# Kernel tuning notes

Hardware: AMD Instinct MI355X
Metric: run time of the kernel (lower is better)

Reference implementation:

```python
import jax, jax.numpy as jnp
import numpy as np

TAU_MIN, TAU_MAX = 5.0, 50.0
BOOST = 3.2
DECO_RATE = 0.01

B, I, F, Q = 4096, 1024, 2048, 4

def setup_inputs() -> dict:
    key = jax.random.key(0)
    ks = jax.random.split(key, 12)
    return {
        "inputs": jax.random.normal(ks[0], (B, I), jnp.float32),
        "hidden_state": jax.random.normal(ks[1], (B, F), jnp.float32),
        "W_in": jax.random.normal(ks[2], (I, F), jnp.float32) / np.sqrt(I),
        "b_in": jnp.zeros((F,), jnp.float32),
        "amp_real": jax.random.normal(ks[3], (F, Q), jnp.float32) * 0.1,
        "amp_imag": jax.random.normal(ks[4], (F, Q), jnp.float32) * 0.1,
        "phase": jax.random.uniform(ks[5], (F, Q), jnp.float32, 0.0, 2 * np.pi),
        "primary": jax.random.normal(ks[6], (F, F), jnp.float32) / np.sqrt(F),
        "ent_mat": jax.random.normal(ks[7], (F, F), jnp.float32) / np.sqrt(F),
        "corr": jax.random.uniform(ks[8], (F,), jnp.float32, 0.0, 0.7),
        "W_tau": jax.random.uniform(ks[9], (F, F), jnp.float32, 0.0, 0.1) / np.sqrt(F),
        "b_tau": jnp.zeros((F,), jnp.float32),
        "W_dec": jax.random.uniform(ks[10], (F, F), jnp.float32, 0.0, 0.5) / np.sqrt(F),
        "b_dec": jnp.zeros((F,), jnp.float32),
        "time_step": 1,
    }

def reference(inputs, hidden_state, W_in, b_in, amp_real, amp_imag, phase,
              primary, ent_mat, corr, W_tau, b_tau, W_dec, b_dec, time_step):
    t = jnp.float32(time_step)
    batch = inputs.shape[0]
    feats = hidden_state.shape[1]

    # input projection: [B,I] @ [I,F]
    x_proj = inputs @ W_in + b_in

    # quantum superposition state (batch-independent, [F,Q] params)
    ph = phase + t * 0.1
    real_c = amp_real * jnp.cos(ph)          # [F,Q]
    imag_c = amp_imag * jnp.sin(ph)          # [F,Q]
    sup_r = real_c.sum(-1)                    # [F]
    sup_i = imag_c.sum(-1)                    # [F]
    prob_amp = real_c ** 2 + imag_c ** 2      # [F,Q]
    q_state = sup_r * jnp.exp(-sup_i ** 2)    # [F]
    q_state_b = jnp.broadcast_to(q_state, (batch, feats))
    prob_amp_b = jnp.broadcast_to(prob_amp, (batch,) + prob_amp.shape)

    # entangled recurrent connections: two F x F matmuls
    ent_rec = hidden_state @ primary + (hidden_state @ ent_mat) * corr

    # quantum time constants
    tau_raw = q_state_b @ W_tau + b_tau
    tau_q = (TAU_MIN + (TAU_MAX - TAU_MIN) * jax.nn.sigmoid(tau_raw)) / BOOST

    # decoherence gate
    deco = jax.nn.sigmoid(q_state_b @ W_dec + b_dec)
    coherent = jnp.exp(-DECO_RATE * t)

    classical = jnp.tanh(x_proj + ent_rec)
    quantum_act = q_state_b * deco * coherent
    combined = classical + quantum_act

    dx_dt = (-hidden_state + combined) / tau_q
    dt_q = 0.1 / BOOST
    new_hidden = hidden_state + dt_q * dx_dt

    # diagnostics
    d_amp = jnp.mean(prob_amp_b, axis=-1)          # [B,F]
    d_coh = coherent
    d_ent = jnp.mean(jnp.abs(ent_rec))
    d_dec = jnp.mean(deco)
    d_tau = jnp.mean(tau_q)
    return (new_hidden, d_amp, d_coh, d_ent, d_dec, d_tau)
```

## Files before the change

kernel.cpp:

```cpp
#include <hip/hip_runtime.h>
#include <hip/hip_bf16.h>

#define BD 4096
#define ID 1024
#define FD 2048

typedef __bf16 v8bf __attribute__((ext_vector_type(8)));
typedef float  v4f  __attribute__((ext_vector_type(4)));

struct alignas(8) bf4 { __hip_bfloat16 x, y, z, w; };

__device__ inline __hip_bfloat16 bf(float f) { return __float2bfloat16(f); }
__device__ inline float sig(float x) { return 1.f / (1.f + expf(-x)); }

__device__ inline void gload16(const __hip_bfloat16* g, __hip_bfloat16* l) {
  __builtin_amdgcn_global_load_lds(
      (const __attribute__((address_space(1))) void*)g,
      (__attribute__((address_space(3))) void*)l, 16, 0, 0);
}

__global__ void k_prep_q(const float* ar, const float* ai, const float* ph,
                         const int* tstep, float* qs, float* pamp,
                         float* scal, float* tau_raw, float* dec_raw) {
  int j = blockIdx.x * 256 + threadIdx.x;
  if (j < 4) scal[j] = 0.f;
  if (j < FD) { tau_raw[j] = 0.f; dec_raw[j] = 0.f; }
  if (j >= FD) return;
  float t = (float)tstep[0];
  float4 a = ((const float4*)ar)[j];
  float4 b = ((const float4*)ai)[j];
  float4 p = ((const float4*)ph)[j];
  float sr = 0.f, si = 0.f, pm = 0.f;
  {
    float c, s, rc, ic;
    c = cosf(p.x + 0.1f * t); s = sinf(p.x + 0.1f * t);
    rc = a.x * c; ic = b.x * s; sr += rc; si += ic; pm += rc * rc + ic * ic;
    c = cosf(p.y + 0.1f * t); s = sinf(p.y + 0.1f * t);
    rc = a.y * c; ic = b.y * s; sr += rc; si += ic; pm += rc * rc + ic * ic;
    c = cosf(p.z + 0.1f * t); s = sinf(p.z + 0.1f * t);
    rc = a.z * c; ic = b.z * s; sr += rc; si += ic; pm += rc * rc + ic * ic;
    c = cosf(p.w + 0.1f * t); s = sinf(p.w + 0.1f * t);
    rc = a.w * c; ic = b.w * s; sr += rc; si += ic; pm += rc * rc + ic * ic;
  }
  qs[j] = sr * expf(-si * si);
  pamp[j] = 0.25f * pm;
}

__global__ void k_cast(const float* s1, __hip_bfloat16* d1, int n1,
                       const float* s2, __hip_bfloat16* d2) {
  int i = blockIdx.x * blockDim.x + threadIdx.x;
  const float* src = s1; __hip_bfloat16* dst = d1;
  if (i >= n1) { i -= n1; src = s2; dst = d2; }
  float4 v = ((const float4*)src)[i];
  bf4 o{bf(v.x), bf(v.y), bf(v.z), bf(v.w)};
  ((bf4*)dst)[i] = o;
}

__global__ void k_tcast(const float* src, const float* src2, const float* corr,
                        __hip_bfloat16* dst, int R, int C, int useM) {
  __shared__ float t[32][33];
  int tx = threadIdx.x, ty = threadIdx.y;
  int x = blockIdx.x * 32 + tx;
  int yb = blockIdx.y * 32;
  float cr = useM ? corr[x] : 0.f;
#pragma unroll
  for (int j = 0; j < 4; j++) {
    int y = yb + ty + j * 8;
    float v = src[(size_t)y * C + x];
    if (useM) v += src2[(size_t)y * C + x] * cr;
    t[ty + j * 8][tx] = v;
  }
  __syncthreads();
#pragma unroll
  for (int j = 0; j < 4; j++) {
    int orow = blockIdx.x * 32 + ty + j * 8;
    int ocol = yb + tx;
    dst[(size_t)orow * R + ocol] = bf(t[tx][ty + j * 8]);
  }
}

__global__ void k_matvec(const float* qs, const float* Wt, const float* Wd,
                         float* tau_raw, float* dec_raw) {
  int j = blockIdx.x * 256 + threadIdx.x;
  int i0 = blockIdx.y * 128;
  const float* W = blockIdx.z ? Wd : Wt;
  float* out = blockIdx.z ? dec_raw : tau_raw;
  __shared__ float q[128];
  if (threadIdx.x < 128) q[threadIdx.x] = qs[i0 + threadIdx.x];
  __syncthreads();
  float acc = 0.f;
#pragma unroll 8
  for (int i = 0; i < 128; i++) acc = fmaf(q[i], W[(size_t)(i0 + i) * FD + j], acc);
  atomicAdd(&out[j], acc);
}

__global__ void k_post(const float* tau_raw, const float* dec_raw, const float* qs,
                       const float* b_tau, const float* b_dec, const int* tstep,
                       float* s_arr, float* qact, float* scal) {
  int j = blockIdx.x * 256 + threadIdx.x;
  float t = (float)tstep[0];
  float coh = expf(-0.01f * t);
  float tq = (5.f + 45.f * sig(tau_raw[j] + b_tau[j])) / 3.2f;
  s_arr[j] = 0.03125f / tq;
  float dec = sig(dec_raw[j] + b_dec[j]);
  qact[j] = qs[j] * dec * coh;
  float tsum = tq, dsum = dec;
  for (int off = 32; off; off >>= 1) {
    tsum += __shfl_down(tsum, off);
    dsum += __shfl_down(dsum, off);
  }
  __shared__ float rt[4], rd[4];
  int w = threadIdx.x >> 6;
  if ((threadIdx.x & 63) == 0) { rt[w] = tsum; rd[w] = dsum; }
  __syncthreads();
  if (threadIdx.x == 0) {
    atomicAdd(&scal[1], rd[0] + rd[1] + rd[2] + rd[3]);
    atomicAdd(&scal[2], rt[0] + rt[1] + rt[2] + rt[3]);
  }
}

__global__ __launch_bounds__(256, 4) void k_gemm_split(
    const __hip_bfloat16* __restrict__ Ah,
    const __hip_bfloat16* __restrict__ MT,
    const __hip_bfloat16* __restrict__ Ax,
    const __hip_bfloat16* __restrict__ WT,
    __hip_bfloat16* __restrict__ g0, __hip_bfloat16* __restrict__ g1,
    __hip_bfloat16* __restrict__ gx) {
  __shared__ alignas(16) __hip_bfloat16 As[2][128][32];
  __shared__ alignas(16) __hip_bfloat16 Bs[2][128][32];

  const int tid = threadIdx.x;
  const int l = tid & 63, w = tid >> 6;
  const int wr = w >> 1, wc = w & 1;
  const int row0 = blockIdx.x * 128, col0 = blockIdx.y * 128;
  const int bz = blockIdx.z;

  const __hip_bfloat16* A = (bz < 2) ? Ah : Ax;
  const __hip_bfloat16* B = (bz < 2) ? MT : WT;
  const int ld = (bz < 2) ? FD : ID;
  const int kb = (bz == 1) ? 1024 : 0;
  __hip_bfloat16* gout = (bz == 0) ? g0 : (bz == 1) ? g1 : gx;

  v4f acc[4][4];
#pragma unroll
  for (int i = 0; i < 4; i++)
#pragma unroll
    for (int j = 0; j < 4; j++) acc[i][j] = (v4f)0.f;

  const int srow = l >> 2;
  const int scol = ((l & 3) ^ ((l >> 3) & 3)) * 8;
  const int rcol = ((l >> 4) ^ ((l >> 1) & 3)) * 8;

  auto stage = [&](int buf, int kt) {
    int k = kb + kt * 32;
#pragma unroll
    for (int i = 0; i < 2; i++) {
      int rr = w * 32 + i * 16;
      gload16(A + (size_t)(row0 + rr + srow) * ld + k + scol, &As[buf][rr][0]);
      gload16(B + (size_t)(col0 + rr + srow) * ld + k + scol, &Bs[buf][rr][0]);
    }
  };
  auto compute = [&](int buf) {
    v8bf a[4], b[4];
#pragma unroll
    for (int mi = 0; mi < 4; mi++)
      a[mi] = *(const v8bf*)&As[buf][wr * 64 + mi * 16 + (l & 15)][rcol];
#pragma unroll
    for (int ni = 0; ni < 4; ni++)
      b[ni] = *(const v8bf*)&Bs[buf][wc * 64 + ni * 16 + (l & 15)][rcol];
#pragma unroll
    for (int mi = 0; mi < 4; mi++)
#pragma unroll
      for (int ni = 0; ni < 4; ni++)
        acc[mi][ni] = __builtin_amdgcn_mfma_f32_16x16x32_bf16(a[mi], b[ni], acc[mi][ni], 0, 0, 0);
  };

  stage(0, 0);
  __syncthreads();
  for (int kt = 0; kt < 32; kt++) {
    if (kt + 1 < 32) stage((kt + 1) & 1, kt + 1);
    compute(kt & 1);
    __syncthreads();
  }

#pragma unroll
  for (int ni = 0; ni < 4; ni++) {
    int gc = col0 + wc * 64 + ni * 16 + (l & 15);
#pragma unroll
    for (int mi = 0; mi < 4; mi++) {
      int gr0 = row0 + wr * 64 + mi * 16 + (l >> 4) * 4;
#pragma unroll
      for (int e = 0; e < 4; e++)
        gout[(size_t)(gr0 + e) * FD + gc] = bf(acc[mi][ni][e]);
    }
  }
}

__global__ __launch_bounds__(256) void k_comb(
    const __hip_bfloat16* __restrict__ g0, const __hip_bfloat16* __restrict__ g1,
    const __hip_bfloat16* __restrict__ gx, const __hip_bfloat16* __restrict__ hbf,
    const float* __restrict__ b_in, const float* __restrict__ s_arr,
    const float* __restrict__ qact, const float* __restrict__ pamp,
    float* __restrict__ entpart, float* __restrict__ out) {
  const int row = blockIdx.x;
  const size_t rb = (size_t)row * FD;
  float asum = 0.f;
#pragma unroll
  for (int half = 0; half < 2; half++) {
    const int c = half * 1024 + threadIdx.x * 4;
    const size_t base = rb + c;
    bf4 e0 = *(const bf4*)(g0 + base);
    bf4 e1 = *(const bf4*)(g1 + base);
    bf4 xx = *(const bf4*)(gx + base);
    bf4 hh = *(const bf4*)(hbf + base);
    float4 bi = *(const float4*)&b_in[c];
    float4 sj = *(const float4*)&s_arr[c];
    float4 qa = *(const float4*)&qact[c];
    float4 pm = *(const float4*)&pamp[c];
    float o[4];
#pragma unroll
    for (int j = 0; j < 4; j++) {
      float e = __bfloat162float((&e0.x)[j]) + __bfloat162float((&e1.x)[j]);
      asum += fabsf(e);
      float g = e + __bfloat162float((&xx.x)[j]) + (&bi.x)[j];
      float comb = tanhf(g) + (&qa.x)[j];
      float h = __bfloat162float((&hh.x)[j]);
      o[j] = fmaf((&sj.x)[j], comb - h, h);
    }
    *(float4*)&out[base] = make_float4(o[0], o[1], o[2], o[3]);
    *(float4*)&out[(size_t)BD * FD + base] = pm;
  }

  for (int off = 32; off; off >>= 1) asum += __shfl_down(asum, off);
  __shared__ float red[4];
  if ((threadIdx.x & 63) == 0) red[threadIdx.x >> 6] = asum;
  __syncthreads();
  if (threadIdx.x == 0)
    entpart[row] = red[0] + red[1] + red[2] + red[3];
}

__global__ void k_fin(const float* __restrict__ entpart, const float* scal,
                      const int* tstep, float* out3) {
  float s = 0.f;
  for (int i = threadIdx.x; i < BD; i += 256) s += entpart[i];
  for (int off = 32; off; off >>= 1) s += __shfl_down(s, off);
  __shared__ float red[4];
  if ((threadIdx.x & 63) == 0) red[threadIdx.x >> 6] = s;
  __syncthreads();
  if (threadIdx.x == 0) {
    float tot = red[0] + red[1] + red[2] + red[3];
    float t = (float)tstep[0];
    out3[0] = expf(-0.01f * t);
    out3[1] = tot / (float)((size_t)BD * FD);
    out3[2] = scal[1] / (float)FD;
    out3[3] = scal[2] / (float)FD;
  }
}

extern "C" void kernel_launch(void* const* d_in, const int* in_sizes, int n_in,
                              void* d_out, int out_size, void* d_ws, size_t ws_size,
                              hipStream_t stream) {
  const float* inputs  = (const float*)d_in[0];
  const float* hidden  = (const float*)d_in[1];
  const float* W_in    = (const float*)d_in[2];
  const float* b_in    = (const float*)d_in[3];
  const float* amp_r   = (const float*)d_in[4];
  const float* amp_i   = (const float*)d_in[5];
  const float* phase   = (const float*)d_in[6];
  const float* primary = (const float*)d_in[7];
  const float* ent_mat = (const float*)d_in[8];
  const float* corr    = (const float*)d_in[9];
  const float* W_tau   = (const float*)d_in[10];
  const float* b_tau   = (const float*)d_in[11];
  const float* W_dec   = (const float*)d_in[12];
  const float* b_dec   = (const float*)d_in[13];
  const int*   tstep   = (const int*)d_in[14];

  char* ws = (char*)d_ws;
  __hip_bfloat16* inputs_bf = (__hip_bfloat16*)(ws + 0);
  __hip_bfloat16* hidden_bf = (__hip_bfloat16*)(ws + 8388608);
  __hip_bfloat16* WT        = (__hip_bfloat16*)(ws + 25165824);
  __hip_bfloat16* MT        = (__hip_bfloat16*)(ws + 29360128);
  __hip_bfloat16* g0        = (__hip_bfloat16*)(ws + 37748736);
  __hip_bfloat16* g1        = (__hip_bfloat16*)(ws + 54525952);
  __hip_bfloat16* gx        = (__hip_bfloat16*)(ws + 71303168);

  char* sb = ws + 88080384;
  float* scal    = (float*)(sb);
  float* qs      = (float*)(sb + 16);
  float* pamp    = (float*)(sb + 16 + 8192);
  float* tau_raw = (float*)(sb + 16 + 2 * 8192);
  float* dec_raw = (float*)(sb + 16 + 3 * 8192);
  float* s_arr   = (float*)(sb + 16 + 4 * 8192);
  float* qact    = (float*)(sb + 16 + 5 * 8192);
  float* entpart = (float*)(sb + 16 + 6 * 8192);

  float* out = (float*)d_out;

  hipLaunchKernelGGL(k_prep_q, dim3(8), dim3(256), 0, stream,
                     amp_r, amp_i, phase, tstep, qs, pamp, scal, tau_raw, dec_raw);
  hipLaunchKernelGGL(k_cast, dim3(12288), dim3(256), 0, stream,
                     inputs, inputs_bf, BD * ID / 4, hidden, hidden_bf);
  hipLaunchKernelGGL(k_tcast, dim3(64, 32), dim3(32, 8), 0, stream,
                     W_in, (const float*)nullptr, (const float*)nullptr, WT, ID, FD, 0);
  hipLaunchKernelGGL(k_tcast, dim3(64, 64), dim3(32, 8), 0, stream,
                     primary, ent_mat, corr, MT, FD, FD, 1);
  hipLaunchKernelGGL(k_matvec, dim3(8, 16, 2), dim3(256), 0, stream, qs, W_tau, W_dec, tau_raw, dec_raw);
  hipLaunchKernelGGL(k_post, dim3(8), dim3(256), 0, stream, tau_raw, dec_raw, qs, b_tau, b_dec, tstep, s_arr, qact, scal);
  hipLaunchKernelGGL(k_gemm_split, dim3(32, 16, 3), dim3(256), 0, stream,
                     hidden_bf, MT, inputs_bf, WT, g0, g1, gx);
  hipLaunchKernelGGL(k_comb, dim3(4096), dim3(256), 0, stream,
                     g0, g1, gx, hidden_bf, b_in, s_arr, qact, pamp, entpart, out);
  hipLaunchKernelGGL(k_fin, dim3(1), dim3(256), 0, stream,
                     entpart, scal, tstep, out + (size_t)2 * BD * FD);
}
```

Before: 143.0 us.

## Fuse prep kernels into one launch and drop split-K GEMM intermediate

Merges the cast, q-state prep, two transpose-casts and the matvec into a single block-indexed kernel. The matvec now recomputes q locally and writes per-slice partials instead of using atomics, and k_post sums those partials. The recurrent GEMM no longer splits K in two with separate bf16 outputs; each block runs the full K=2048, so one 16MB intermediate write and read disappears and k_comb loads one fewer tensor. The trade-off is that the GEMM grid shrinks from 1536 to 1024 blocks, with longer-running blocks in the recurrent half, which may leave the load unevenly balanced across CUs.

Result: faster. 125.8 us (median of 2 runs) (-12.1%).

```diff
diff --git a/kernel.cpp b/kernel.cpp
--- a/kernel.cpp
+++ b/kernel.cpp
@@ -19,90 +19,126 @@
       (__attribute__((address_space(3))) void*)l, 16, 0, 0);
 }
 
-__global__ void k_prep_q(const float* ar, const float* ai, const float* ph,
-                         const int* tstep, float* qs, float* pamp,
-                         float* scal, float* tau_raw, float* dec_raw) {
+#define MB_CAST  12288
+#define MB_PREP  (MB_CAST + 8)
+#define MB_TCW   (MB_PREP + 2048)
+#define MB_TCM   (MB_TCW + 4096)
+#define MB_MV    (MB_TCM + 256)
+
+__global__ void k_mega(
+    const float* __restrict__ inputs, const float* __restrict__ hidden,
+    const float* __restrict__ W_in, const float* __restrict__ primary,
+    const float* __restrict__ ent_mat, const float* __restrict__ corr,
+    const float* __restrict__ W_tau, const float* __restrict__ W_dec,
+    const float* __restrict__ ar, const float* __restrict__ ai,
+    const float* __restrict__ ph, const int* __restrict__ tstep,
+    __hip_bfloat16* __restrict__ inputs_bf, __hip_bfloat16* __restrict__ hidden_bf,
+    __hip_bfloat16* __restrict__ WT, __hip_bfloat16* __restrict__ MT,
+    float* __restrict__ qs, float* __restrict__ pamp,
+    float* __restrict__ ptau, float* __restrict__ pdec) {
+  __shared__ float tbuf[32][33];
+  __shared__ float q[128];
+  const int b = blockIdx.x, tid = threadIdx.x;
+
+  if (b < MB_CAST) {
+    int i = b * 256 + tid;
+    const float* src = inputs; __hip_bfloat16* dst = inputs_bf;
+    int n1 = BD * ID / 4;
+    if (i >= n1) { i -= n1; src = hidden; dst = hidden_bf; }
+    float4 v = ((const float4*)src)[i];
+    bf4 o{bf(v.x), bf(v.y), bf(v.z), bf(v.w)};
+    ((bf4*)dst)[i] = o;
+
+  } else if (b < MB_PREP) {
+    int j = (b - MB_CAST) * 256 + tid;
+    float t = (float)tstep[0];
+    float4 a = ((const float4*)ar)[j];
+    float4 bb = ((const float4*)ai)[j];
+    float4 p = ((const float4*)ph)[j];
+    float sr = 0.f, si = 0.f, pm = 0.f;
+#pragma unroll
+    for (int k = 0; k < 4; k++) {
+      float pk = (&p.x)[k] + 0.1f * t;
+      float rc = (&a.x)[k] * cosf(pk), ic = (&bb.x)[k] * sinf(pk);
+      sr += rc; si += ic; pm += rc * rc + ic * ic;
+    }
+    qs[j] = sr * expf(-si * si);
+    pamp[j] = 0.25f * pm;
+
+  } else if (b < MB_TCM) {
+    int isM = (b >= MB_TCW);
+    int b2 = b - (isM ? MB_TCW : MB_PREP);
+    const float* src = isM ? primary : W_in;
+    const float* src2 = ent_mat;
+    __hip_bfloat16* dst = isM ? MT : WT;
+    int C = FD, R = isM ? FD : ID;
+    int tx = tid & 31, ty = tid >> 5;
+    int x = (b2 & 63) * 32 + tx;
+    int yb = (b2 >> 6) * 32;
+    float cr = isM ? corr[x] : 0.f;
+#pragma unroll
+    for (int j = 0; j < 4; j++) {
+      int y = yb + ty + j * 8;
+      float v = src[(size_t)y * C + x];
+      if (isM) v += src2[(size_t)y * C + x] * cr;
+      tbuf[ty + j * 8][tx] = v;
+    }
+    __syncthreads();
+#pragma unroll
+    for (int j = 0; j < 4; j++) {
+      int orow = (b2 & 63) * 32 + ty + j * 8;
+      int ocol = yb + tx;
+      dst[(size_t)orow * R + ocol] = bf(tbuf[tx][ty + j * 8]);
+    }
+
+  } else {
+    int b2 = b - MB_TCM;
+    int jb = b2 & 7, p = (b2 >> 3) & 15, z = b2 >> 7;
+    int i0 = p * 128;
+    if (tid < 128) {
+      int i = i0 + tid;
+      float t = (float)tstep[0];
+      float4 a = ((const float4*)ar)[i];
+      float4 bb = ((const float4*)ai)[i];
+      float4 pp = ((const float4*)ph)[i];
+      float sr = 0.f, si = 0.f;
+#pragma unroll
+      for (int k = 0; k < 4; k++) {
+        float pk = (&pp.x)[k] + 0.1f * t;
+        sr += (&a.x)[k] * cosf(pk);
+        si += (&bb.x)[k] * sinf(pk);
+      }
+      q[tid] = sr * expf(-si * si);
+    }
+    __syncthreads();
+    const float* W = z ? W_dec : W_tau;
+    float* outp = z ? pdec : ptau;
+    int j = jb * 256 + tid;
+    float acc = 0.f;
+#pragma unroll 8
+    for (int i = 0; i < 128; i++)
+      acc = fmaf(q[i], W[(size_t)(i0 + i) * FD + j], acc);
+    outp[p * FD + j] = acc;
+  }
+}
+
+__global__ void k_post(const float* __restrict__ ptau, const float* __restrict__ pdec,
+                       const float* __restrict__ qs, const float* __restrict__ b_tau,
+                       const float* __restrict__ b_dec, const int* tstep,
+                       float* __restrict__ s_arr, float* __restrict__ qact,
+                       float* __restrict__ tpart, float* __restrict__ dpart) {
   int j = blockIdx.x * 256 + threadIdx.x;
-  if (j < 4) scal[j] = 0.f;
-  if (j < FD) { tau_raw[j] = 0.f; dec_raw[j] = 0.f; }
-  if (j >= FD) return;
-  float t = (float)tstep[0];
-  float4 a = ((const float4*)ar)[j];
-  float4 b = ((const float4*)ai)[j];
-  float4 p = ((const float4*)ph)[j];
-  float sr = 0.f, si = 0.f, pm = 0.f;
-  {
-    float c, s, rc, ic;
-    c = cosf(p.x + 0.1f * t); s = sinf(p.x + 0.1f * t);
-    rc = a.x * c; ic = b.x * s; sr += rc; si += ic; pm += rc * rc + ic * ic;
-    c = cosf(p.y + 0.1f * t); s = sinf(p.y + 0.1f * t);
-    rc = a.y * c; ic = b.y * s; sr += rc; si += ic; pm += rc * rc + ic * ic;
-    c = cosf(p.z + 0.1f * t); s = sinf(p.z + 0.1f * t);
-    rc = a.z * c; ic = b.z * s; sr += rc; si += ic; pm += rc * rc + ic * ic;
-    c = cosf(p.w + 0.1f * t); s = sinf(p.w + 0.1f * t);
-    rc = a.w * c; ic = b.w * s; sr += rc; si += ic; pm += rc * rc + ic * ic;
-  }
-  qs[j] = sr * expf(-si * si);
-  pamp[j] = 0.25f * pm;
-}
-
-__global__ void k_cast(const float* s1, __hip_bfloat16* d1, int n1,
-                       const float* s2, __hip_bfloat16* d2) {
-  int i = blockIdx.x * blockDim.x + threadIdx.x;
-  const float* src = s1; __hip_bfloat16* dst = d1;
-  if (i >= n1) { i -= n1; src = s2; dst = d2; }
-  float4 v = ((const float4*)src)[i];
-  bf4 o{bf(v.x), bf(v.y), bf(v.z), bf(v.w)};
-  ((bf4*)dst)[i] = o;
-}
-
-__global__ void k_tcast(const float* src, const float* src2, const float* corr,
-                        __hip_bfloat16* dst, int R, int C, int useM) {
-  __shared__ float t[32][33];
-  int tx = threadIdx.x, ty = threadIdx.y;
-  int x = blockIdx.x * 32 + tx;
-  int yb = blockIdx.y * 32;
-  float cr = useM ? corr[x] : 0.f;
-#pragma unroll
-  for (int j = 0; j < 4; j++) {
-    int y = yb + ty + j * 8;
-    float v = src[(size_t)y * C + x];
-    if (useM) v += src2[(size_t)y * C + x] * cr;
-    t[ty + j * 8][tx] = v;
-  }
-  __syncthreads();
-#pragma unroll
-  for (int j = 0; j < 4; j++) {
-    int orow = blockIdx.x * 32 + ty + j * 8;
-    int ocol = yb + tx;
-    dst[(size_t)orow * R + ocol] = bf(t[tx][ty + j * 8]);
-  }
-}
-
-__global__ void k_matvec(const float* qs, const float* Wt, const float* Wd,
-                         float* tau_raw, float* dec_raw) {
-  int j = blockIdx.x * 256 + threadIdx.x;
-  int i0 = blockIdx.y * 128;
-  const float* W = blockIdx.z ? Wd : Wt;
-  float* out = blockIdx.z ? dec_raw : tau_raw;
-  __shared__ float q[128];
-  if (threadIdx.x < 128) q[threadIdx.x] = qs[i0 + threadIdx.x];
-  __syncthreads();
-  float acc = 0.f;
-#pragma unroll 8
-  for (int i = 0; i < 128; i++) acc = fmaf(q[i], W[(size_t)(i0 + i) * FD + j], acc);
-  atomicAdd(&out[j], acc);
-}
-
-__global__ void k_post(const float* tau_raw, const float* dec_raw, const float* qs,
-                       const float* b_tau, const float* b_dec, const int* tstep,
-                       float* s_arr, float* qact, float* scal) {
-  int j = blockIdx.x * 256 + threadIdx.x;
+  float tr = b_tau[j], dr = b_dec[j];
+#pragma unroll
+  for (int p = 0; p < 16; p++) {
+    tr += ptau[p * FD + j];
+    dr += pdec[p * FD + j];
+  }
   float t = (float)tstep[0];
   float coh = expf(-0.01f * t);
-  float tq = (5.f + 45.f * sig(tau_raw[j] + b_tau[j])) / 3.2f;
+  float tq = (5.f + 45.f * sig(tr)) / 3.2f;
   s_arr[j] = 0.03125f / tq;
-  float dec = sig(dec_raw[j] + b_dec[j]);
+  float dec = sig(dr);
   qact[j] = qs[j] * dec * coh;
   float tsum = tq, dsum = dec;
   for (int off = 32; off; off >>= 1) {
@@ -114,18 +150,17 @@
   if ((threadIdx.x & 63) == 0) { rt[w] = tsum; rd[w] = dsum; }
   __syncthreads();
   if (threadIdx.x == 0) {
-    atomicAdd(&scal[1], rd[0] + rd[1] + rd[2] + rd[3]);
-    atomicAdd(&scal[2], rt[0] + rt[1] + rt[2] + rt[3]);
-  }
-}
-
-__global__ __launch_bounds__(256, 4) void k_gemm_split(
+    tpart[blockIdx.x] = rt[0] + rt[1] + rt[2] + rt[3];
+    dpart[blockIdx.x] = rd[0] + rd[1] + rd[2] + rd[3];
+  }
+}
+
+__global__ __launch_bounds__(256, 4) void k_gemm2(
     const __hip_bfloat16* __restrict__ Ah,
     const __hip_bfloat16* __restrict__ MT,
     const __hip_bfloat16* __restrict__ Ax,
     const __hip_bfloat16* __restrict__ WT,
-    __hip_bfloat16* __restrict__ g0, __hip_bfloat16* __restrict__ g1,
-    __hip_bfloat16* __restrict__ gx) {
+    __hip_bfloat16* __restrict__ ge, __hip_bfloat16* __restrict__ gx) {
   __shared__ alignas(16) __hip_bfloat16 As[2][128][32];
   __shared__ alignas(16) __hip_bfloat16 Bs[2][128][32];
 
@@ -135,11 +170,11 @@
   const int row0 = blockIdx.x * 128, col0 = blockIdx.y * 128;
   const int bz = blockIdx.z;
 
-  const __hip_bfloat16* A = (bz < 2) ? Ah : Ax;
-  const __hip_bfloat16* B = (bz < 2) ? MT : WT;
-  const int ld = (bz < 2) ? FD : ID;
-  const int kb = (bz == 1) ? 1024 : 0;
-  __hip_bfloat16* gout = (bz == 0) ? g0 : (bz == 1) ? g1 : gx;
+  const __hip_bfloat16* A = bz ? Ax : Ah;
+  const __hip_bfloat16* B = bz ? WT : MT;
+  const int ld = bz ? ID : FD;
+  const int nkt = bz ? 32 : 64;
+  __hip_bfloat16* gout = bz ? gx : ge;
 
   v4f acc[4][4];
 #pragma unroll
@@ -152,7 +187,7 @@
   const int rcol = ((l >> 4) ^ ((l >> 1) & 3)) * 8;
 
   auto stage = [&](int buf, int kt) {
-    int k = kb + kt * 32;
+    int k = kt * 32;
 #pragma unroll
     for (int i = 0; i < 2; i++) {
       int rr = w * 32 + i * 16;
@@ -177,8 +212,8 @@
 
   stage(0, 0);
   __syncthreads();
-  for (int kt = 0; kt < 32; kt++) {
-    if (kt + 1 < 32) stage((kt + 1) & 1, kt + 1);
+  for (int kt = 0; kt < nkt; kt++) {
+    if (kt + 1 < nkt) stage((kt + 1) & 1, kt + 1);
     compute(kt & 1);
     __syncthreads();
   }
@@ -197,8 +232,8 @@
 }
 
 __global__ __launch_bounds__(256) void k_comb(
-    const __hip_bfloat16* __restrict__ g0, const __hip_bfloat16* __restrict__ g1,
-    const __hip_bfloat16* __restrict__ gx, const __hip_bfloat16* __restrict__ hbf,
+    const __hip_bfloat16* __restrict__ ge, const __hip_bfloat16* __restrict__ gx,
+    const __hip_bfloat16* __restrict__ hbf,
     const float* __restrict__ b_in, const float* __restrict__ s_arr,
     const float* __restrict__ qact, const float* __restrict__ pamp,
     float* __restrict__ entpart, float* __restrict__ out) {
@@ -209,8 +244,7 @@
   for (int half = 0; half < 2; half++) {
     const int c = half * 1024 + threadIdx.x * 4;
     const size_t base = rb + c;
-    bf4 e0 = *(const bf4*)(g0 + base);
-    bf4 e1 = *(const bf4*)(g1 + base);
+    bf4 e0 = *(const bf4*)(ge + base);
     bf4 xx = *(const bf4*)(gx + base);
     bf4 hh = *(const bf4*)(hbf + base);
     float4 bi = *(const float4*)&b_in[c];
@@ -220,7 +254,7 @@
     float o[4];
 #pragma unroll
     for (int j = 0; j < 4; j++) {
-      float e = __bfloat162float((&e0.x)[j]) + __bfloat162float((&e1.x)[j]);
+      float e = __bfloat162float((&e0.x)[j]);
       asum += fabsf(e);
       float g = e + __bfloat162float((&xx.x)[j]) + (&bi.x)[j];
       float comb = tanhf(g) + (&qa.x)[j];
@@ -239,8 +273,8 @@
     entpart[row] = red[0] + red[1] + red[2] + red[3];
 }
 
-__global__ void k_fin(const float* __restrict__ entpart, const float* scal,
-                      const int* tstep, float* out3) {
+__global__ void k_fin(const float* __restrict__ entpart, const float* __restrict__ tpart,
+                      const float* __restrict__ dpart, const int* tstep, float* out3) {
   float s = 0.f;
   for (int i = threadIdx.x; i < BD; i += 256) s += entpart[i];
   for (int off = 32; off; off >>= 1) s += __shfl_down(s, off);
@@ -249,11 +283,14 @@
   __syncthreads();
   if (threadIdx.x == 0) {
     float tot = red[0] + red[1] + red[2] + red[3];
+    float ts = 0.f, ds = 0.f;
+#pragma unroll
+    for (int i = 0; i < 8; i++) { ts += tpart[i]; ds += dpart[i]; }
     float t = (float)tstep[0];
     out3[0] = expf(-0.01f * t);
     out3[1] = tot / (float)((size_t)BD * FD);
-    out3[2] = scal[1] / (float)FD;
-    out3[3] = scal[2] / (float)FD;
+    out3[2] = ds / (float)FD;
+    out3[3] = ts / (float)FD;
   }
 }
 
@@ -281,36 +318,32 @@
   __hip_bfloat16* hidden_bf = (__hip_bfloat16*)(ws + 8388608);
   __hip_bfloat16* WT        = (__hip_bfloat16*)(ws + 25165824);
   __hip_bfloat16* MT        = (__hip_bfloat16*)(ws + 29360128);
-  __hip_bfloat16* g0        = (__hip_bfloat16*)(ws + 37748736);
-  __hip_bfloat16* g1        = (__hip_bfloat16*)(ws + 54525952);
-  __hip_bfloat16* gx        = (__hip_bfloat16*)(ws + 71303168);
-
-  char* sb = ws + 88080384;
-  float* scal    = (float*)(sb);
-  float* qs      = (float*)(sb + 16);
-  float* pamp    = (float*)(sb + 16 + 8192);
-  float* tau_raw = (float*)(sb + 16 + 2 * 8192);
-  float* dec_raw = (float*)(sb + 16 + 3 * 8192);
-  float* s_arr   = (float*)(sb + 16 + 4 * 8192);
-  float* qact    = (float*)(sb + 16 + 5 * 8192);
-  float* entpart = (float*)(sb + 16 + 6 * 8192);
+  __hip_bfloat16* ge        = (__hip_bfloat16*)(ws + 37748736);
+  __hip_bfloat16* gx        = (__hip_bfloat16*)(ws + 54525952);
+
+  char* sb = ws + 71303168;
+  float* qs      = (float*)(sb);
+  float* pamp    = (float*)(sb + 8192);
+  float* s_arr   = (float*)(sb + 2 * 8192);
+  float* qact    = (float*)(sb + 3 * 8192);
+  float* ptau    = (float*)(sb + 4 * 8192);
+  float* pdec    = (float*)(sb + 4 * 8192 + 131072);
+  float* entpart = (float*)(sb + 4 * 8192 + 262144);
+  float* tpart   = (float*)(sb + 4 * 8192 + 278528);
+  float* dpart   = (float*)(sb + 4 * 8192 + 278528 + 64);
 
   float* out = (float*)d_out;
 
-  hipLaunchKernelGGL(k_prep_q, dim3(8), dim3(256), 0, stream,
-                     amp_r, amp_i, phase, tstep, qs, pamp, scal, tau_raw, dec_raw);
-  hipLaunchKernelGGL(k_cast, dim3(12288), dim3(256), 0, stream,
-                     inputs, inputs_bf, BD * ID / 4, hidden, hidden_bf);
-  hipLaunchKernelGGL(k_tcast, dim3(64, 32), dim3(32, 8), 0, stream,
-                     W_in, (const float*)nullptr, (const float*)nullptr, WT, ID, FD, 0);
-  hipLaunchKernelGGL(k_tcast, dim3(64, 64), dim3(32, 8), 0, stream,
-                     primary, ent_mat, corr, MT, FD, FD, 1);
-  hipLaunchKernelGGL(k_matvec, dim3(8, 16, 2), dim3(256), 0, stream, qs, W_tau, W_dec, tau_raw, dec_raw);
-  hipLaunchKernelGGL(k_post, dim3(8), dim3(256), 0, stream, tau_raw, dec_raw, qs, b_tau, b_dec, tstep, s_arr, qact, scal);
-  hipLaunchKernelGGL(k_gemm_split, dim3(32, 16, 3), dim3(256), 0, stream,
-                     hidden_bf, MT, inputs_bf, WT, g0, g1, gx);
+  hipLaunchKernelGGL(k_mega, dim3(MB_MV), dim3(256), 0, stream,
+                     inputs, hidden, W_in, primary, ent_mat, corr, W_tau, W_dec,
+                     amp_r, amp_i, phase, tstep,
+                     inputs_bf, hidden_bf, WT, MT, qs, pamp, ptau, pdec);
+  hipLaunchKernelGGL(k_post, dim3(8), dim3(256), 0, stream,
+                     ptau, pdec, qs, b_tau, b_dec, tstep, s_arr, qact, tpart, dpart);
+  hipLaunchKernelGGL(k_gemm2, dim3(32, 16, 2), dim3(256), 0, stream,
+                     hidden_bf, MT, inputs_bf, WT, ge, gx);
   hipLaunchKernelGGL(k_comb, dim3(4096), dim3(256), 0, stream,
-                     g0, g1, gx, hidden_bf, b_in, s_arr, qact, pamp, entpart, out);
+                     ge, gx, hidden_bf, b_in, s_arr, qact, pamp, entpart, out);
   hipLaunchKernelGGL(k_fin, dim3(1), dim3(256), 0, stream,
-                     entpart, scal, tstep, out + (size_t)2 * BD * FD);
-}
+                     entpart, tpart, dpart, tstep, out + (size_t)2 * BD * FD);
+}
```
